# Performance work log

Measured on AMD Instinct MI355X. Metric: run time of the kernel, lower is better.

The kernel has to match this reference:

```python
import jax, jax.numpy as jnp
import numpy as np

S, N, LAT, HID, NH, NLAYERS = 8, 128, 128, 384, 8, 6
HT, WT, DT = 128, 128, 128
DIN, DOUT, RAD, LEVELS, FED = 1169, 3 + 3 * 128, 3, 4, 64


def sincos1d(d, pos):
    # MAE-style 1d sincos embedding, d even -> [..., d]
    omega = 1.0 / (10000.0 ** (jnp.arange(d // 2, dtype=jnp.float32) / (d / 2.0)))
    ang = pos[..., None] * omega
    return jnp.concatenate([jnp.sin(ang), jnp.cos(ang)], axis=-1)


def flow_embed(f, Cd=FED):
    # get_3d_embedding(flows, 64, cat_coords=True) -> [..., 3*Cd+3] = 195
    div = jnp.arange(0, Cd, 2, dtype=jnp.float32) * (1000.0 / Cd)
    outs = []
    for a in range(3):
        ang = f[..., a, None] * div
        pe = jnp.stack([jnp.sin(ang), jnp.cos(ang)], axis=-1).reshape(f.shape[:-1] + (Cd,))
        outs.append(pe)
    return jnp.concatenate(outs + [f], axis=-1)


def avg_pool2(x):
    B, Sv, Cc, H, W = x.shape
    return x.reshape(B, Sv, Cc, H // 2, 2, W // 2, 2).mean(axis=(4, 6))


def pyramid(fm):
    pyr = [fm]
    for _ in range(LEVELS - 1):
        fm = avg_pool2(fm)
        pyr.append(fm)
    return pyr


def bilinear_sample(corr, xy):
    # corr: [B,S,N,H,W]; xy: [B,S,N,P,2] pixel coords (x indexes W, y indexes H); zero padding
    B, Sv, Nn, H, W = corr.shape
    cf = corr.reshape(B, Sv, Nn, H * W)
    x, y = xy[..., 0], xy[..., 1]
    x0f = jnp.floor(x); y0f = jnp.floor(y)
    wx, wy = x - x0f, y - y0f
    x0 = x0f.astype(jnp.int32); y0 = y0f.astype(jnp.int32)

    def gather(xi, yi):
        ok = ((xi >= 0) & (xi < W) & (yi >= 0) & (yi < H)).astype(cf.dtype)
        idx = jnp.clip(yi, 0, H - 1) * W + jnp.clip(xi, 0, W - 1)
        v = jnp.take_along_axis(cf, idx.reshape(B, Sv, Nn, -1), axis=-1).reshape(idx.shape)
        return v * ok

    v00 = gather(x0, y0); v01 = gather(x0 + 1, y0)
    v10 = gather(x0, y0 + 1); v11 = gather(x0 + 1, y0 + 1)
    return v00 * (1 - wx) * (1 - wy) + v01 * wx * (1 - wy) + v10 * (1 - wx) * wy + v11 * wx * wy


def corr_sample(pyr, targets, coords):
    # RAFT/CoTracker CorrBlock: per-level dense correlation then (2r+1)^2 window bilinear lookup
    d = jnp.arange(-RAD, RAD + 1, dtype=jnp.float32)
    delta = jnp.stack(jnp.meshgrid(d, d, indexing="ij"), axis=-1).reshape(-1, 2)  # [49,2]
    scale = 1.0 / jnp.sqrt(jnp.float32(targets.shape[-1]))
    outs = []
    for l, fm in enumerate(pyr):
        corr = jnp.einsum("bsnc,bschw->bsnhw", targets, fm) * scale
        xy = coords[..., None, :] / (2.0 ** l) + delta
        outs.append(bilinear_sample(corr, xy))
    return jnp.concatenate(outs, axis=-1)  # [B,S,N,196]


def layernorm(x, g, b):
    m = x.mean(-1, keepdims=True)
    v = x.var(-1, keepdims=True)
    return (x - m) / jnp.sqrt(v + 1e-5) * g + b


def attention(x, Wqkv, bq, Wo, bo):
    M, T, H = x.shape
    dh = H // NH
    qkv = (x @ Wqkv + bq).reshape(M, T, 3, NH, dh)
    q, k, v = qkv[:, :, 0], qkv[:, :, 1], qkv[:, :, 2]
    att = jax.nn.softmax(jnp.einsum("mthd,mshd->mhts", q, k) / jnp.sqrt(jnp.float32(dh)), axis=-1)
    o = jnp.einsum("mhts,mshd->mthd", att, v).reshape(M, T, H)
    return o @ Wo + bo


def updateformer(x, support, W_in, b_in, lnp, Wqkv, bqkv, Wo, bo, W1, b1, W2, b2, W_out, b_out, Ws, bs):
    # x: [B,N,T,DIN]; alternating time (over T) and space (over N) pre-LN transformer blocks
    B, Np, T, _ = x.shape
    sproj = support @ Ws + bs  # [100,HID]
    h = x @ W_in + b_in + sproj.mean(axis=0)
    for i in range(NLAYERS):
        g1, bb1, g2, bb2 = lnp[i, 0], lnp[i, 1], lnp[i, 2], lnp[i, 3]
        if i % 2 == 0:
            y = h.reshape(B * Np, T, HID)
        else:
            y = h.transpose(0, 2, 1, 3).reshape(B * T, Np, HID)
        y = y + attention(layernorm(y, g1, bb1), Wqkv[i], bqkv[i], Wo[i], bo[i])
        z = layernorm(y, g2, bb2)
        y = y + jax.nn.gelu(z @ W1[i] + b1[i], approximate=False) @ W2[i] + b2[i]
        if i % 2 == 0:
            h = y.reshape(B, Np, T, HID)
        else:
            h = y.reshape(B, T, Np, HID).transpose(0, 2, 1, 3)
    return h @ W_out + b_out, sproj[None]


def groupnorm1(x, g, b):
    m = x.mean(-1, keepdims=True)
    v = x.var(-1, keepdims=True)
    return (x - m) / jnp.sqrt(v + 1e-5) * g + b


def _forward(fmapXY, fmapYZ, fmapXZ, coords_init, vis_init, track_mask, feat_init, support_features,
             W_in, b_in, lnp, Wqkv, bqkv, Wo, bo, W1, b1, W2, b2, W_out, b_out, Ws, bs,
             gn_g, gn_b, Wu, bu, Wvis, bvis, iters):
    B, Sv, Cc, H, W = fmapXY.shape
    D = fmapXZ.shape[-2]
    Nn = coords_init.shape[2]
    coords = coords_init
    ffeats = [feat_init[..., k] for k in range(3)]
    pyrXY, pyrYZ, pyrXZ = pyramid(fmapXY), pyramid(fmapYZ), pyramid(fmapXZ)
    grid_size = jnp.array([H, W, D], dtype=jnp.float32)
    # 3d sincos pos embed from query coords; 1169 padded to 1170 -> 390/axis, truncated back
    g = (coords[:, 0] / grid_size * 2.0 - 1.0) * 128.0  # [B,N,3]
    pe = jnp.concatenate([sincos1d(390, g[..., i]) for i in range(3)], axis=-1)[..., :DIN]
    pos_embed = pe.reshape(B * Nn, 1, DIN)
    times_embed = sincos1d(1170, jnp.arange(Sv, dtype=jnp.float32))[None, :, :DIN]
    support = support_features
    for _ in range(iters):
        coords = jax.lax.stop_gradient(coords)  # matches coords.detach()
        fxy = corr_sample(pyrXY, ffeats[0], coords[..., :2])
        fyz = corr_sample(pyrYZ, ffeats[1], coords[..., 1:3])
        fxz = corr_sample(pyrXZ, ffeats[2], coords[..., 0::2])
        fcorrs = jnp.concatenate([fxy, fyz, fxz], axis=-1)  # [B,S,N,588]
        fcorrs_ = fcorrs.transpose(0, 2, 1, 3).reshape(B * Nn, Sv, -1)
        flows_ = (coords - coords[:, :1]).transpose(0, 2, 1, 3).reshape(B * Nn, Sv, 3)
        flows_cat = flow_embed(flows_)  # [BN,S,195]
        ff = [f.transpose(0, 2, 1, 3).reshape(B * Nn, Sv, LAT) for f in ffeats]
        ffeats_ = jnp.concatenate(ff, axis=-1)  # [BN,S,384]
        # replicate torch's cat(dim=2)+permute+reshape layout exactly
        tmv = jnp.concatenate([track_mask, vis_init], axis=2).transpose(0, 2, 1, 3).reshape(B * Nn, Sv, 2)
        tin = jnp.concatenate([flows_cat, fcorrs_, ffeats_, tmv], axis=-1)  # [BN,S,1169]
        x = (tin + pos_embed + times_embed).reshape(B, Nn, Sv, DIN)
        delta, dse3 = updateformer(x, support, W_in, b_in, lnp, Wqkv, bqkv, Wo, bo, W1, b1, W2, b2, W_out, b_out, Ws, bs)
        support = support + dse3[0] / 100.0
        delta = delta.reshape(B * Nn, Sv, DOUT)
        d_coord = delta[..., :3].reshape(B, Nn, Sv, 3).transpose(0, 2, 1, 3)
        coords = coords + d_coord
        new_ffeats = []
        for k in range(3):
            dfk = delta[..., 3 + k * LAT:3 + (k + 1) * LAT]
            upd = jax.nn.gelu(groupnorm1(dfk, gn_g[k], gn_b[k]) @ Wu[k] + bu[k], approximate=False)
            new_ffeats.append(ffeats[k] + upd.reshape(B, Nn, Sv, LAT).transpose(0, 2, 1, 3))
        ffeats = new_ffeats
    vis = (jnp.concatenate(ffeats, axis=-1) @ Wvis + bvis)[..., 0]  # [B,S,N]
    return jnp.concatenate([coords, vis[..., None]], axis=-1)  # [B,S,N,4]


def setup_inputs() -> dict:
    key = jax.random.key(0)
    ks = jax.random.split(key, 16)
    f32 = jnp.float32
    B = 1
    fmapXY = jax.random.normal(ks[0], (B, S, LAT, HT, WT), f32)
    fmapYZ = jax.random.normal(ks[1], (B, S, LAT, DT, HT), f32)
    fmapXZ = jax.random.normal(ks[2], (B, S, LAT, DT, WT), f32)
    coords_init = jax.random.uniform(ks[3], (B, S, N, 3), f32) * 112.0 + 8.0
    vis_init = jnp.ones((B, S, N, 1), f32)
    track_mask = jnp.ones((B, S, N, 1), f32)
    feat_init = jax.random.normal(ks[4], (B, S, N, LAT, 3), f32)
    support_features = jnp.zeros((100, HID), f32) + 0.1
    w = lambda k, sh: jax.random.normal(k, sh, f32) * 0.02
    ln1 = jnp.stack([jnp.ones(HID, f32), jnp.zeros(HID, f32), jnp.ones(HID, f32), jnp.zeros(HID, f32)])
    params = dict(
        W_in=w(ks[5], (DIN, HID)), b_in=jnp.zeros((HID,), f32),
        lnp=jnp.tile(ln1[None], (NLAYERS, 1, 1)),
        Wqkv=w(ks[6], (NLAYERS, HID, 3 * HID)), bqkv=jnp.zeros((NLAYERS, 3 * HID), f32),
        Wo=w(ks[7], (NLAYERS, HID, HID)), bo=jnp.zeros((NLAYERS, HID), f32),
        W1=w(ks[8], (NLAYERS, HID, 4 * HID)), b1=jnp.zeros((NLAYERS, 4 * HID), f32),
        W2=w(ks[9], (NLAYERS, 4 * HID, HID)), b2=jnp.zeros((NLAYERS, HID), f32),
        W_out=w(ks[10], (HID, DOUT)), b_out=jnp.zeros((DOUT,), f32),
        Ws=w(ks[11], (HID, HID)), bs=jnp.zeros((HID,), f32),
        gn_g=jnp.ones((3, LAT), f32), gn_b=jnp.zeros((3, LAT), f32),
        Wu=w(ks[12], (3, LAT, LAT)), bu=jnp.zeros((3, LAT), f32),
        Wvis=w(ks[13], (3 * LAT, 1)), bvis=jnp.zeros((1,), f32),
    )
    return dict(fmapXY=fmapXY, fmapYZ=fmapYZ, fmapXZ=fmapXZ, coords_init=coords_init,
                vis_init=vis_init, track_mask=track_mask, feat_init=feat_init,
                support_features=support_features, iters=2, **params)


def reference(fmapXY, fmapYZ, fmapXZ, coords_init, vis_init, track_mask, feat_init, support_features,
              W_in, b_in, lnp, Wqkv, bqkv, Wo, bo, W1, b1, W2, b2, W_out, b_out, Ws, bs,
              gn_g, gn_b, Wu, bu, Wvis, bvis, iters):
    return _forward(fmapXY, fmapYZ, fmapXZ, coords_init, vis_init, track_mask, feat_init, support_features,
                    W_in, b_in, lnp, Wqkv, bqkv, Wo, bo, W1, b1, W2, b2, W_out, b_out, Ws, bs,
                    gn_g, gn_b, Wu, bu, Wvis, bvis, iters)
```

## Files before the change

kernel.cpp:

```cpp
#include <hip/hip_runtime.h>
#include <hip/hip_bf16.h>


#define DEVFN __device__ __forceinline__

typedef __attribute__((ext_vector_type(8))) short short8;
typedef __attribute__((ext_vector_type(4))) float f32x4;

static constexpr float INV_SQRT_DH = 0.14433756729740643f;
static constexpr float CORR_SCALE  = 0.08838834764831845f;
static constexpr size_t VSTRIDE = 22282240;

DEVFN float gelu_exact(float x){
  return 0.5f * x * (1.0f + erff(x * 0.7071067811865476f));
}
DEVFN short bf16_of(float f){
  __hip_bfloat16 b = __float2bfloat16(f);
  return *reinterpret_cast<short*>(&b);
}
DEVFN float bfu(uint32_t u16){ return __uint_as_float(u16 << 16); }
DEVFN float bf2f(__hip_bfloat16 b){ return __bfloat162float(b); }

DEVFN f32x4 MFMA(short8 a, short8 b, f32x4 c){
  return __builtin_amdgcn_mfma_f32_16x16x32_bf16(a,b,c,0,0,0);
}

template<int K, int MODE, bool AF32, int DEPTH>
static __device__ void mgemm_body(int bx, int by, const void* __restrict__ A, int lda,
                                  const __hip_bfloat16* __restrict__ Bt,
                                  float* __restrict__ C, int ldc,
                                  int M, int N, const float* __restrict__ bias, int tid){
  constexpr int NSTEP = K/32;
  int lane = tid & 63, wid = tid >> 6;
  int wr = wid >> 1, wc = wid & 1;
  int lr = lane & 15, lk = lane >> 4;
  int m0 = by*64 + wr*32;
  int n0 = bx*64 + wc*32;

  const __hip_bfloat16* Ab = (const __hip_bfloat16*)A;
  const float* Af = (const float*)A;
  size_t arow0 = (size_t)(m0 + lr)      * lda;
  size_t arow1 = (size_t)(m0 + 16 + lr) * lda;
  size_t brow0 = (size_t)(n0 + lr)      * K;
  size_t brow1 = (size_t)(n0 + 16 + lr) * K;

  auto loadA = [&](size_t ro, int k0)->short8{
    if constexpr (AF32){
      const float* p = Af + ro + k0 + lk*8;
      short8 r;
      #pragma unroll
      for (int j=0;j<8;j++) r[j] = bf16_of(p[j]);
      return r;
    } else {
      return *reinterpret_cast<const short8*>(Ab + ro + k0 + lk*8);
    }
  };
  auto loadB = [&](size_t ro, int k0)->short8{
    return *reinterpret_cast<const short8*>(Bt + ro + k0 + lk*8);
  };

  short8 a0[DEPTH], a1[DEPTH], b0[DEPTH], b1[DEPTH];
  #pragma unroll
  for (int p=0;p<DEPTH;p++){
    if (p < NSTEP){
      a0[p]=loadA(arow0,p*32); a1[p]=loadA(arow1,p*32);
      b0[p]=loadB(brow0,p*32); b1[p]=loadB(brow1,p*32);
    }
  }
  f32x4 acc00 = {}, acc01 = {}, acc10 = {}, acc11 = {};
  #pragma unroll
  for (int t=0;t<NSTEP;t++){
    const int cur = t % DEPTH;
    acc00 = MFMA(a0[cur],b0[cur],acc00);
    acc01 = MFMA(a0[cur],b1[cur],acc01);
    acc10 = MFMA(a1[cur],b0[cur],acc10);
    acc11 = MFMA(a1[cur],b1[cur],acc11);
    if (t+DEPTH < NSTEP){
      int k0 = (t+DEPTH)*32;
      a0[cur]=loadA(arow0,k0); a1[cur]=loadA(arow1,k0);
      b0[cur]=loadB(brow0,k0); b1[cur]=loadB(brow1,k0);
    }
  }

  f32x4 accs[2][2] = {{acc00, acc01},{acc10, acc11}};
  #pragma unroll
  for (int mi=0;mi<2;mi++){
    #pragma unroll
    for (int ni=0;ni<2;ni++){
      int c = n0 + ni*16 + lr;
      if (c >= N) continue;
      float bv = bias ? bias[c] : 0.0f;
      #pragma unroll
      for (int reg=0;reg<4;reg++){
        int r = m0 + mi*16 + lk*4 + reg;
        if (r >= M) continue;
        float v = accs[mi][ni][reg] + bv;
        if (MODE==0) C[(size_t)r*ldc + c] = v;
        else C[(size_t)r*ldc + c] += v;
      }
    }
  }
}

__global__ void init_all_k(float* coords, const float* cinit,
                           float* ff, const float* feat_init,
                           float* support, const float* sfeat,
                           float* posE, float* timE){
  int idx = blockIdx.x*256 + threadIdx.x;
  if (idx < 3072)  coords[idx]  = cinit[idx];
  if (idx < 49152){
    int row = idx / 384;
    support[idx] = (row < 100) ? sfeat[idx] : 0.0f;
  }
  if (idx < 393216){
    int k = idx / 131072, rest = idx % 131072;
    ff[idx] = feat_init[(size_t)rest*3 + k];
  }
  if (idx < 149632){
    int n = idx / 1169, d = idx % 1169;
    int i = d / 390, dd = d % 390;
    float c = cinit[n*3 + i];
    float g = (c / 128.0f * 2.0f - 1.0f) * 128.0f;
    int m = (dd < 195) ? dd : dd - 195;
    float om = powf(10000.0f, -(float)m / 195.0f);
    float ang = g * om;
    posE[idx] = (dd < 195) ? sinf(ang) : cosf(ang);
  }
  if (idx < 9352){
    int s = idx / 1169, d = idx % 1169;
    int m = (d < 585) ? d : d - 585;
    float om = powf(10000.0f, -(float)m / 585.0f);
    float ang = (float)s * om;
    timE[idx] = (d < 585) ? sinf(ang) : cosf(ang);
  }
}

__global__ void transpose_cl_k(const float* __restrict__ inXY, const float* __restrict__ inYZ,
                               const float* __restrict__ inXZ, __hip_bfloat16* __restrict__ pyr){
  __shared__ float tile[32][129];
  int v = blockIdx.z >> 3, s = blockIdx.z & 7;
  const float* in = (v==0) ? inXY : ((v==1) ? inYZ : inXZ);
  int c0 = blockIdx.y*32, h0 = blockIdx.x*128;
  int tx = threadIdx.x & 31, ty = threadIdx.x >> 5;
  const float* ib = in + (size_t)s*128*16384;
  #pragma unroll
  for (int r=0;r<4;r++){
    int c = c0 + ty + r*8;
    float4 f = *reinterpret_cast<const float4*>(ib + (size_t)c*16384 + h0 + tx*4);
    tile[ty+r*8][tx*4+0]=f.x; tile[ty+r*8][tx*4+1]=f.y;
    tile[ty+r*8][tx*4+2]=f.z; tile[ty+r*8][tx*4+3]=f.w;
  }
  __syncthreads();
  __hip_bfloat16* ob = pyr + (size_t)v*VSTRIDE + (size_t)s*16384*128;
  #pragma unroll
  for (int rr=0;rr<16;rr++){
    int hw = ty + rr*8;
    ob[(size_t)(h0+hw)*128 + c0 + tx] = __float2bfloat16(tile[tx][hw]);
  }
}

__global__ void pool2_k(__hip_bfloat16* __restrict__ pyr, size_t in_off, size_t out_off, int So){
  int idx = blockIdx.x*256 + threadIdx.x;
  int total = 8*So*So*128;
  if (idx >= total) return;
  const __hip_bfloat16* in = pyr + (size_t)blockIdx.z*VSTRIDE + in_off;
  __hip_bfloat16* out      = pyr + (size_t)blockIdx.z*VSTRIDE + out_off;
  int c = idx & 127;
  int x = (idx >> 7) % So;
  int y = ((idx >> 7) / So) % So;
  int s = idx / (So*So*128);
  int Si = So*2;
  const __hip_bfloat16* b0 = in + (((size_t)s*Si + 2*y)*Si + 2*x)*128 + c;
  float v = bf2f(b0[0]) + bf2f(b0[128])
          + bf2f(b0[(size_t)Si*128]) + bf2f(b0[(size_t)Si*128 + 128]);
  out[idx] = __float2bfloat16(v*0.25f);
}

__global__ void wtrans_all_k(const float* Ws, const float* W_in, const float* Wqkv,
                             const float* Wo, const float* W1, const float* W2,
                             const float* W_out, const float* Wu,
                             __hip_bfloat16* WsT, __hip_bfloat16* WinT, __hip_bfloat16* WqkvT,
                             __hip_bfloat16* WoT, __hip_bfloat16* W1T, __hip_bfloat16* W2T,
                             __hip_bfloat16* WoutT, __hip_bfloat16* WuT){
  __shared__ float tile[32][33];
  int z = blockIdx.z;
  const float* in; __hip_bfloat16* out; int K,N,Kp,Np;
  if (z==0){ in=Ws; out=WsT; K=384;N=384;Kp=384;Np=384; }
  else if (z==1){ in=W_in; out=WinT; K=1169;N=384;Kp=1184;Np=384; }
  else if (z<8){ int l=z-2; in=Wqkv+(size_t)l*442368; out=WqkvT+(size_t)l*442368; K=384;N=1152;Kp=384;Np=1152; }
  else if (z<14){ int l=z-8; in=Wo+(size_t)l*147456; out=WoT+(size_t)l*147456; K=384;N=384;Kp=384;Np=384; }
  else if (z<20){ int l=z-14; in=W1+(size_t)l*589824; out=W1T+(size_t)l*589824; K=384;N=1536;Kp=384;Np=1536; }
  else if (z<26){ int l=z-20; in=W2+(size_t)l*589824; out=W2T+(size_t)l*589824; K=1536;N=384;Kp=1536;Np=384; }
  else if (z==26){ in=W_out; out=WoutT; K=384;N=387;Kp=384;Np=448; }
  else { int l=z-27; in=Wu+(size_t)l*16384; out=WuT+(size_t)l*16384; K=128;N=128;Kp=128;Np=128; }
  int MK = (K>Kp)?K:Kp, MN = (N>Np)?N:Np;
  int kb = blockIdx.y*32, nb = blockIdx.x*32;
  if (kb >= MK || nb >= MN) return;
  int tx = threadIdx.x & 31, ty = threadIdx.x >> 5;
  #pragma unroll
  for (int r=0;r<4;r++){
    int k = kb + ty + r*8, n = nb + tx;
    tile[ty+r*8][tx] = (k < K && n < N) ? in[(size_t)k*N + n] : 0.0f;
  }
  __syncthreads();
  #pragma unroll
  for (int r=0;r<4;r++){
    int n = nb + ty + r*8, k = kb + tx;
    if (n < Np && k < Kp) out[(size_t)n*Kp + k] = __float2bfloat16(tile[tx][ty+r*8]);
  }
}

__global__ void assemble_x_k(__hip_bfloat16* __restrict__ xbuf, const float* __restrict__ posE,
                             const float* __restrict__ timE, const float* __restrict__ coords,
                             const float* __restrict__ ff, const float* __restrict__ tmask,
                             const float* __restrict__ vinit,
                             const float* __restrict__ support,
                             const __hip_bfloat16* __restrict__ WsT,
                             float* __restrict__ sproj, const float* __restrict__ bs){
  if (blockIdx.x >= 1024){
    int b = blockIdx.x - 1024;
    mgemm_body<384,0,true,3>(b%6, b/6, support,384, WsT, sproj,384, 100,384, bs, threadIdx.x);
    return;
  }
  int r = blockIdx.x;
  int n = r >> 3, s = r & 7;
  for (int d = threadIdx.x; d < 1184; d += blockDim.x){
    __hip_bfloat16* dst = xbuf + (size_t)r*1184 + d;
    if (d >= 1169){ *dst = __float2bfloat16(0.0f); continue; }
    float base = posE[(size_t)n*1169 + d] + timE[(size_t)s*1169 + d];
    if (d >= 195 && d < 783){ *dst = __float2bfloat16(base); continue; }
    float val;
    if (d < 195){
      if (d >= 192){
        int a = d - 192;
        val = coords[(s*128+n)*3 + a] - coords[n*3 + a];
      } else {
        int a = d >> 6, dd = d & 63;
        float f = coords[(s*128+n)*3 + a] - coords[n*3 + a];
        float ang = f * (31.25f * (float)(dd >> 1));
        val = (dd & 1) ? cosf(ang) : sinf(ang);
      }
    } else if (d < 1167){
      int cidx = d - 783, k = cidx >> 7, cc = cidx & 127;
      val = ff[(size_t)k*131072 + (size_t)(s*128+n)*128 + cc];
    } else {
      int c = d - 1167;
      int flat = n*16 + s*2 + c;
      int n2 = flat >> 3, s2 = flat & 7;
      val = (n2 < 128) ? tmask[s2*128 + n2] : vinit[s2*128 + (n2-128)];
    }
    *dst = __float2bfloat16(val + base);
  }
}

__global__ void corr_k(const __hip_bfloat16* __restrict__ pyr, const float* __restrict__ coords,
                       const float* __restrict__ ff, __hip_bfloat16* __restrict__ xbuf,
                       const float* __restrict__ sproj, const float* __restrict__ b_in,
                       float* __restrict__ bias2, float* __restrict__ support){
  if (blockIdx.x >= 3072){
    int idx = (blockIdx.x - 3072)*256 + threadIdx.x;
    if (idx < 38400) support[idx] += sproj[idx]*0.01f;
    else if (idx < 38784){
      int c = idx - 38400;
      float s = 0.0f;
      for (int r=0;r<100;r++) s += sproj[r*384 + c];
      bias2[c] = b_in[c] + s*0.01f;
    }
    return;
  }
  __shared__ float t[128];
  __shared__ float p[4][64];
  int bid = blockIdx.x;
  int view = bid >> 10, s = (bid >> 7) & 7, n = bid & 127;
  int tid = threadIdx.x;
  int l = tid >> 6, t64 = tid & 63;
  if (tid < 128) t[tid] = ff[(size_t)view*131072 + (size_t)(s*128+n)*128 + tid];
  int ax = (view==1) ? 1 : 0;
  int ay = (view==0) ? 1 : 2;
  float X = coords[(s*128+n)*3 + ax];
  float Y = coords[(s*128+n)*3 + ay];
  const __hip_bfloat16* vb = pyr + (size_t)view*VSTRIDE;
  __syncthreads();

  int sz = 128 >> l;
  size_t loff = (l==0) ? 0ull : (l==1 ? 16777216ull : (l==2 ? 20971520ull : 22020096ull));
  float inv = 1.0f / (float)(1 << l);
  float cx = X * inv, cy = Y * inv;
  float x0f = floorf(cx), y0f = floorf(cy);
  float wx = cx - x0f, wy = cy - y0f;
  int ix0 = (int)x0f, iy0 = (int)y0f;
  int px = ix0 - 3 + (t64 & 7);
  int py = iy0 - 3 + (t64 >> 3);
  float acc = 0.0f;
  if (px >= 0 && px < sz && py >= 0 && py < sz){
    const uint2* row = reinterpret_cast<const uint2*>(vb + loff + (((size_t)s*sz + py)*sz + px)*128);
    #pragma unroll
    for (int c4=0;c4<32;c4++){
      uint2 u = row[c4];
      float f0 = __uint_as_float(u.x << 16);
      float f1 = __uint_as_float(u.x & 0xffff0000u);
      float f2 = __uint_as_float(u.y << 16);
      float f3 = __uint_as_float(u.y & 0xffff0000u);
      acc += t[c4*4+0]*f0 + t[c4*4+1]*f1 + t[c4*4+2]*f2 + t[c4*4+3]*f3;
    }
  }
  p[l][t64] = acc;
  __syncthreads();
  if (t64 < 49){
    int i = t64 / 7, jj = t64 % 7;
    float v = p[l][jj*8+i]       * (1.0f-wx)*(1.0f-wy)
            + p[l][jj*8+i+1]     * wx*(1.0f-wy)
            + p[l][(jj+1)*8+i]   * (1.0f-wx)*wy
            + p[l][(jj+1)*8+i+1] * wx*wy;
    __hip_bfloat16* dst = xbuf + (size_t)(n*8+s)*1184 + 195 + view*196 + l*49 + t64;
    *dst = __float2bfloat16(__bfloat162float(*dst) + v * CORR_SCALE);
  }
}

__global__ void gn_rows_k(const float* __restrict__ dbuf,
                          const float* __restrict__ gn_g, const float* __restrict__ gn_b,
                          __hip_bfloat16* __restrict__ gtmp, float* __restrict__ coords){
  int k = blockIdx.y;
  const float* in = dbuf + 3 + k*128;
  const float* g = gn_g + k*128;
  const float* b = gn_b + k*128;
  __hip_bfloat16* out = gtmp + (size_t)k*131072;
  int wave = threadIdx.x >> 6, lane = threadIdx.x & 63;
  int r = blockIdx.x*4 + wave;
  const float* row = in + (size_t)r*387;
  float x0 = row[lane], x1 = row[lane+64];
  float sum = x0 + x1;
  #pragma unroll
  for (int o=32;o>0;o>>=1) sum += __shfl_xor(sum, o);
  float mean = sum / 128.0f;
  float d0 = x0-mean, d1 = x1-mean;
  float vs = d0*d0 + d1*d1;
  #pragma unroll
  for (int o=32;o>0;o>>=1) vs += __shfl_xor(vs, o);
  float invstd = 1.0f / sqrtf(vs/128.0f + 1e-5f);
  out[(size_t)r*128 + lane]      = __float2bfloat16(d0*invstd*g[lane] + b[lane]);
  out[(size_t)r*128 + lane + 64] = __float2bfloat16(d1*invstd*g[lane+64] + b[lane+64]);
  if (k == 0 && blockIdx.x < 12){
    int idx = blockIdx.x*256 + threadIdx.x;
    if (idx < 3072){
      int a = idx % 3, sn = idx / 3;
      int ss = sn >> 7, nn = sn & 127;
      coords[idx] += dbuf[(size_t)(nn*8+ss)*387 + a];
    }
  }
}

template<int K, int MODE, bool AF32, int DEPTH>
__global__ __launch_bounds__(256) void mgemm_k(const void* __restrict__ A, int lda,
                                               const __hip_bfloat16* __restrict__ Bt,
                                               float* __restrict__ C, int ldc,
                                               int M, int N,
                                               const float* __restrict__ bias){
  mgemm_body<K,MODE,AF32,DEPTH>(blockIdx.x, blockIdx.y, A, lda, Bt, C, ldc, M, N, bias, threadIdx.x);
}

__global__ __launch_bounds__(256) void ln_qkv_k(const float* __restrict__ A,
                                                const float* __restrict__ gamma,
                                                const float* __restrict__ beta,
                                                const __hip_bfloat16* __restrict__ Bt,
                                                __hip_bfloat16* __restrict__ Cbf,
                                                const float* __restrict__ bias){
  constexpr int LDSS = 392;
  __shared__ short Asm[64*LDSS];
  int tid = threadIdx.x, lane = tid & 63, w = tid >> 6;
  int m0 = blockIdx.y*64, n0b = blockIdx.x*128;

  float gg[6], bb[6];
  #pragma unroll
  for (int e=0;e<6;e++){ gg[e] = gamma[lane+e*64]; bb[e] = beta[lane+e*64]; }
  for (int rr=0; rr<16; rr++){
    int r = w*16 + rr;
    const float* row = A + (size_t)(m0+r)*384;
    float x[6]; float sum = 0.0f;
    #pragma unroll
    for (int e=0;e<6;e++){ x[e] = row[lane+e*64]; sum += x[e]; }
    #pragma unroll
    for (int o=32;o>0;o>>=1) sum += __shfl_xor(sum, o);
    float mean = sum * (1.0f/384.0f);
    float vs = 0.0f;
    #pragma unroll
    for (int e=0;e<6;e++){ float d = x[e]-mean; vs += d*d; }
    #pragma unroll
    for (int o=32;o>0;o>>=1) vs += __shfl_xor(vs, o);
    float invstd = 1.0f / sqrtf(vs*(1.0f/384.0f) + 1e-5f);
    #pragma unroll
    for (int e=0;e<6;e++)
      Asm[r*LDSS + lane + e*64] = bf16_of((x[e]-mean)*invstd*gg[e] + bb[e]);
  }
  __syncthreads();

  int wr = w >> 1, wc = w & 1;
  int lr = lane & 15, lk = lane >> 4;
  const __hip_bfloat16* Brow[4];
  #pragma unroll
  for (int ni=0;ni<4;ni++) Brow[ni] = Bt + (size_t)(n0b + wc*64 + ni*16 + lr)*384;

  short8 bfrag[4][4];
  #pragma unroll
  for (int p=0;p<4;p++)
    #pragma unroll
    for (int ni=0;ni<4;ni++)
      bfrag[p][ni] = *(const short8*)(Brow[ni] + p*32 + lk*8);

  f32x4 acc[2][4] = {};
  #pragma unroll
  for (int t=0;t<12;t++){
    const int cur = t & 3;
    short8 a0 = *(const short8*)(&Asm[(wr*32+lr)*LDSS    + t*32 + lk*8]);
    short8 a1 = *(const short8*)(&Asm[(wr*32+16+lr)*LDSS + t*32 + lk*8]);
    #pragma unroll
    for (int ni=0;ni<4;ni++){
      acc[0][ni] = MFMA(a0,bfrag[cur][ni],acc[0][ni]);
      acc[1][ni] = MFMA(a1,bfrag[cur][ni],acc[1][ni]);
    }
    if (t+4 < 12){
      #pragma unroll
      for (int ni=0;ni<4;ni++)
        bfrag[cur][ni] = *(const short8*)(Brow[ni] + (t+4)*32 + lk*8);
    }
  }
  #pragma unroll
  for (int mi=0;mi<2;mi++){
    #pragma unroll
    for (int ni=0;ni<4;ni++){
      int c = n0b + wc*64 + ni*16 + lr;
      float bv = bias[c];
      #pragma unroll
      for (int reg=0;reg<4;reg++){
        int r = m0 + wr*32 + mi*16 + lk*4 + reg;
        Cbf[(size_t)r*1152 + c] = __float2bfloat16(acc[mi][ni][reg] + bv);
      }
    }
  }
}

template<bool GELU>
__global__ __launch_bounds__(256) void lngemm_k(const float* __restrict__ A,
                                                const float* __restrict__ gamma,
                                                const float* __restrict__ beta,
                                                const __hip_bfloat16* __restrict__ Bt,
                                                __hip_bfloat16* __restrict__ Cbf, int ldc,
                                                const float* __restrict__ bias){
  constexpr int LDSS = 392;
  __shared__ short Asm[64*LDSS];
  int tid = threadIdx.x, lane = tid & 63, w = tid >> 6;
  int m0 = blockIdx.y*64, n0b = blockIdx.x*128;

  float gg[6], bb[6];
  #pragma unroll
  for (int e=0;e<6;e++){ gg[e] = gamma[lane+e*64]; bb[e] = beta[lane+e*64]; }
  for (int rr=0; rr<16; rr++){
    int r = w*16 + rr;
    const float* row = A + (size_t)(m0+r)*384;
    float x[6]; float sum = 0.0f;
    #pragma unroll
    for (int e=0;e<6;e++){ x[e] = row[lane+e*64]; sum += x[e]; }
    #pragma unroll
    for (int o=32;o>0;o>>=1) sum += __shfl_xor(sum, o);
    float mean = sum * (1.0f/384.0f);
    float vs = 0.0f;
    #pragma unroll
    for (int e=0;e<6;e++){ float d = x[e]-mean; vs += d*d; }
    #pragma unroll
    for (int o=32;o>0;o>>=1) vs += __shfl_xor(vs, o);
    float invstd = 1.0f / sqrtf(vs*(1.0f/384.0f) + 1e-5f);
    #pragma unroll
    for (int e=0;e<6;e++)
      Asm[r*LDSS + lane + e*64] = bf16_of((x[e]-mean)*invstd*gg[e] + bb[e]);
  }
  __syncthreads();

  int wr = w >> 1, wc = w & 1;
  int lr = lane & 15, lk = lane >> 4;
  const __hip_bfloat16* Brow[4];
  #pragma unroll
  for (int ni=0;ni<4;ni++) Brow[ni] = Bt + (size_t)(n0b + wc*64 + ni*16 + lr)*384;

  short8 bfrag[2][4];
  #pragma unroll
  for (int p=0;p<2;p++)
    #pragma unroll
    for (int ni=0;ni<4;ni++)
      bfrag[p][ni] = *(const short8*)(Brow[ni] + p*32 + lk*8);

  f32x4 acc[2][4] = {};
  #pragma unroll
  for (int t=0;t<12;t++){
    const int cur = t & 1;
    short8 a0 = *(const short8*)(&Asm[(wr*32+lr)*LDSS    + t*32 + lk*8]);
    short8 a1 = *(const short8*)(&Asm[(wr*32+16+lr)*LDSS + t*32 + lk*8]);
    #pragma unroll
    for (int ni=0;ni<4;ni++){
      acc[0][ni] = MFMA(a0,bfrag[cur][ni],acc[0][ni]);
      acc[1][ni] = MFMA(a1,bfrag[cur][ni],acc[1][ni]);
    }
    if (t+2 < 12){
      #pragma unroll
      for (int ni=0;ni<4;ni++)
        bfrag[cur][ni] = *(const short8*)(Brow[ni] + (t+2)*32 + lk*8);
    }
  }
  #pragma unroll
  for (int mi=0;mi<2;mi++){
    #pragma unroll
    for (int ni=0;ni<4;ni++){
      int c = n0b + wc*64 + ni*16 + lr;
      float bv = bias[c];
      #pragma unroll
      for (int reg=0;reg<4;reg++){
        int r = m0 + wr*32 + mi*16 + lk*4 + reg;
        float v = acc[mi][ni][reg] + bv;
        Cbf[(size_t)r*ldc + c] = __float2bfloat16(GELU ? gelu_exact(v) : v);
      }
    }
  }
}

__global__ __launch_bounds__(256) void wu_gemm_k(const __hip_bfloat16* __restrict__ gtmp,
                                                 const __hip_bfloat16* __restrict__ WuT,
                                                 const float* __restrict__ bu,
                                                 float* __restrict__ ff){
  int z = blockIdx.z;
  const __hip_bfloat16* A  = gtmp + (size_t)z*131072;
  const __hip_bfloat16* Bt = WuT  + (size_t)z*16384;
  const float* bias = bu + (size_t)z*128;
  float* aux = ff + (size_t)z*131072;
  int tid = threadIdx.x, lane = tid & 63, wid = tid >> 6;
  int wr = wid >> 1, wc = wid & 1;
  int lr = lane & 15, lk = lane >> 4;
  int m0 = blockIdx.y*64 + wr*32;
  int n0 = blockIdx.x*64 + wc*32;
  const short8* A0 = (const short8*)(A + (size_t)(m0+lr)*128);
  const short8* A1 = (const short8*)(A + (size_t)(m0+16+lr)*128);
  const short8* B0 = (const short8*)(Bt + (size_t)(n0+lr)*128);
  const short8* B1 = (const short8*)(Bt + (size_t)(n0+16+lr)*128);
  f32x4 acc00={}, acc01={}, acc10={}, acc11={};
  #pragma unroll
  for (int t=0;t<4;t++){
    short8 a0 = A0[t*4 + lk], a1 = A1[t*4 + lk];
    short8 b0 = B0[t*4 + lk], b1 = B1[t*4 + lk];
    acc00 = MFMA(a0,b0,acc00);
    acc01 = MFMA(a0,b1,acc01);
    acc10 = MFMA(a1,b0,acc10);
    acc11 = MFMA(a1,b1,acc11);
  }
  f32x4 accs[2][2] = {{acc00, acc01},{acc10, acc11}};
  #pragma unroll
  for (int mi=0;mi<2;mi++){
    #pragma unroll
    for (int ni=0;ni<2;ni++){
      int c = n0 + ni*16 + lr;
      float bv = bias[c];
      #pragma unroll
      for (int reg=0;reg<4;reg++){
        int r = m0 + mi*16 + lk*4 + reg;
        float v = accs[mi][ni][reg] + bv;
        int ss = r & 7, nn2 = r >> 3;
        aux[((size_t)(ss*128+nn2))*128 + c] += gelu_exact(v);
      }
    }
  }
}

__global__ __launch_bounds__(512) void attn_even_k(const __hip_bfloat16* __restrict__ qkv,
                                                   __hip_bfloat16* __restrict__ attout){
  int g = blockIdx.x;
  int h = threadIdx.x >> 6;
  int lane = threadIdx.x & 63;
  int t = lane >> 3, j = lane & 7;
  const short* qs = (const short*)qkv;

  float q[48], kk[48];
  {
    const short8* qp = (const short8*)(qs + (size_t)(g*8+t)*1152 + h*48);
    const short8* kp = (const short8*)(qs + (size_t)(g*8+j)*1152 + 384 + h*48);
    #pragma unroll
    for (int c=0;c<6;c++){
      short8 qv = qp[c], kv = kp[c];
      #pragma unroll
      for (int e=0;e<8;e++){
        q[c*8+e]  = bfu((uint16_t)qv[e]);
        kk[c*8+e] = bfu((uint16_t)kv[e]);
      }
    }
  }
  float s = 0.0f;
  #pragma unroll
  for (int d=0;d<48;d++) s += q[d]*kk[d];
  s *= INV_SQRT_DH;
  float mx = s;
  #pragma unroll
  for (int o=1;o<8;o<<=1) mx = fmaxf(mx, __shfl_xor(mx, o));
  float e = expf(s - mx);
  float l = e;
  #pragma unroll
  for (int o=1;o<8;o<<=1) l += __shfl_xor(l, o);
  float p = e / l;

  float o6[6] = {0,0,0,0,0,0};
  #pragma unroll
  for (int jp=0;jp<8;jp++){
    float pj = __shfl(p, (lane & 56) | jp);
    const uint32_t* vp = (const uint32_t*)(qs + (size_t)(g*8+jp)*1152 + 768 + h*48 + j*6);
    uint32_t w0 = vp[0], w1 = vp[1], w2 = vp[2];
    o6[0] += pj * bfu(w0 & 0xffffu); o6[1] += pj * bfu(w0 >> 16);
    o6[2] += pj * bfu(w1 & 0xffffu); o6[3] += pj * bfu(w1 >> 16);
    o6[4] += pj * bfu(w2 & 0xffffu); o6[5] += pj * bfu(w2 >> 16);
  }
  uint32_t r0 = ((uint32_t)(uint16_t)bf16_of(o6[1]) << 16) | (uint16_t)bf16_of(o6[0]);
  uint32_t r1 = ((uint32_t)(uint16_t)bf16_of(o6[3]) << 16) | (uint16_t)bf16_of(o6[2]);
  uint32_t r2 = ((uint32_t)(uint16_t)bf16_of(o6[5]) << 16) | (uint16_t)bf16_of(o6[4]);
  uint32_t* op = (uint32_t*)((short*)attout + (size_t)(g*8+t)*384 + h*48 + j*6);
  op[0] = r0; op[1] = r1; op[2] = r2;
}

__global__ __launch_bounds__(256) void attn_odd_mfma_k(const __hip_bfloat16* __restrict__ qkv,
                                                       __hip_bfloat16* __restrict__ attout){
  __shared__ char smem[47872];
  short* Qb = (short*)smem;
  short* Kb = (short*)(smem + 18432);
  short* Pb = (short*)smem;
  short* Vt = (short*)(smem + 34816);
  int g = blockIdx.x & 7, h = blockIdx.x >> 3;
  int tid = threadIdx.x;

  const short* qs = (const short*)qkv;
  for (int idx = tid; idx < 768; idx += 256){
    int t = idx / 6, dblk = idx % 6;
    size_t base = (size_t)(t*8+g)*1152 + h*48 + dblk*8;
    *(short8*)(Qb + t*72 + dblk*8) = *(const short8*)(qs + base);
    *(short8*)(Kb + t*72 + dblk*8) = *(const short8*)(qs + base + 384);
  }
  short8 zz = {};
  for (int idx = tid; idx < 384; idx += 256){
    int t = idx / 3, dblk = idx % 3;
    *(short8*)(Qb + t*72 + 48 + dblk*8) = zz;
    *(short8*)(Kb + t*72 + 48 + dblk*8) = zz;
  }
  __syncthreads();

  int lane = tid & 63, w = tid >> 6;
  int lr = lane & 15, lk = lane >> 4;
  int m0 = w*32;

  f32x4 S[2][8] = {};
  #pragma unroll
  for (int ks=0; ks<2; ks++){
    short8 a0 = *(const short8*)(Qb + (m0+lr)*72    + ks*32 + lk*8);
    short8 a1 = *(const short8*)(Qb + (m0+16+lr)*72 + ks*32 + lk*8);
    #pragma unroll
    for (int ni=0; ni<8; ni++){
      short8 b = *(const short8*)(Kb + (ni*16+lr)*72 + ks*32 + lk*8);
      S[0][ni] = MFMA(a0,b,S[0][ni]);
      S[1][ni] = MFMA(a1,b,S[1][ni]);
    }
  }

  #pragma unroll
  for (int mi=0;mi<2;mi++){
    #pragma unroll
    for (int reg=0;reg<4;reg++){
      float m = -1e30f;
      #pragma unroll
      for (int ni=0;ni<8;ni++) m = fmaxf(m, S[mi][ni][reg]);
      #pragma unroll
      for (int o=1;o<16;o<<=1) m = fmaxf(m, __shfl_xor(m, o));
      m *= INV_SQRT_DH;
      float l = 0.0f;
      #pragma unroll
      for (int ni=0;ni<8;ni++){
        float p = expf(S[mi][ni][reg]*INV_SQRT_DH - m);
        S[mi][ni][reg] = p;
        l += p;
      }
      #pragma unroll
      for (int o=1;o<16;o<<=1) l += __shfl_xor(l, o);
      float inv = 1.0f/l;
      #pragma unroll
      for (int ni=0;ni<8;ni++) S[mi][ni][reg] *= inv;
    }
  }
  __syncthreads();

  for (int idx = tid; idx < 768; idx += 256){
    int j = idx / 6, dblk = idx % 6;
    short8 v = *(const short8*)(qs + (size_t)(j*8+g)*1152 + 768 + h*48 + dblk*8);
    #pragma unroll
    for (int e=0;e<8;e++) Vt[(dblk*8+e)*136 + j] = v[e];
  }
  #pragma unroll
  for (int mi=0;mi<2;mi++)
    #pragma unroll
    for (int ni=0;ni<8;ni++)
      #pragma unroll
      for (int reg=0;reg<4;reg++)
        Pb[(m0+mi*16+lk*4+reg)*136 + ni*16+lr] = bf16_of(S[mi][ni][reg]);
  __syncthreads();

  f32x4 O[2][3] = {};
  #pragma unroll
  for (int ks=0; ks<4; ks++){
    short8 a0 = *(const short8*)(Pb + (m0+lr)*136    + ks*32 + lk*8);
    short8 a1 = *(const short8*)(Pb + (m0+16+lr)*136 + ks*32 + lk*8);
    #pragma unroll
    for (int ni=0; ni<3; ni++){
      short8 b = *(const short8*)(Vt + (ni*16+lr)*136 + ks*32 + lk*8);
      O[0][ni] = MFMA(a0,b,O[0][ni]);
      O[1][ni] = MFMA(a1,b,O[1][ni]);
    }
  }
  #pragma unroll
  for (int mi=0;mi<2;mi++){
    #pragma unroll
    for (int ni=0;ni<3;ni++){
      #pragma unroll
      for (int reg=0;reg<4;reg++){
        int q = m0 + mi*16 + lk*4 + reg;
        int d = ni*16 + lr;
        attout[(size_t)(q*8+g)*384 + h*48 + d] = __float2bfloat16(O[mi][ni][reg]);
      }
    }
  }
}

__global__ void final_out_k(const float* __restrict__ coords, const float* __restrict__ ff,
                            const float* __restrict__ Wvis, const float* __restrict__ bvis,
                            float* __restrict__ out){
  int sn = blockIdx.x*64 + threadIdx.x;
  if (sn >= 1024) return;
  float acc = bvis[0];
  for (int k=0;k<3;k++)
    for (int c=0;c<128;c++)
      acc += ff[(size_t)k*131072 + (size_t)sn*128 + c] * Wvis[k*128 + c];
  out[sn*4+0] = coords[sn*3+0];
  out[sn*4+1] = coords[sn*3+1];
  out[sn*4+2] = coords[sn*3+2];
  out[sn*4+3] = acc;
}


extern "C" void kernel_launch(void* const* d_in, const int* in_sizes, int n_in,
                              void* d_out, int out_size, void* d_ws, size_t ws_size,
                              hipStream_t stream) {
  const float* fmapXY   = (const float*)d_in[0];
  const float* fmapYZ   = (const float*)d_in[1];
  const float* fmapXZ   = (const float*)d_in[2];
  const float* cinit    = (const float*)d_in[3];
  const float* vinit    = (const float*)d_in[4];
  const float* tmask    = (const float*)d_in[5];
  const float* feat_init= (const float*)d_in[6];
  const float* sfeat    = (const float*)d_in[7];
  const float* W_in     = (const float*)d_in[9];
  const float* b_in     = (const float*)d_in[10];
  const float* lnp      = (const float*)d_in[11];
  const float* Wqkv     = (const float*)d_in[12];
  const float* bqkv     = (const float*)d_in[13];
  const float* Wo       = (const float*)d_in[14];
  const float* bo       = (const float*)d_in[15];
  const float* W1       = (const float*)d_in[16];
  const float* b1       = (const float*)d_in[17];
  const float* W2       = (const float*)d_in[18];
  const float* b2       = (const float*)d_in[19];
  const float* W_out    = (const float*)d_in[20];
  const float* b_out    = (const float*)d_in[21];
  const float* Ws       = (const float*)d_in[22];
  const float* bs       = (const float*)d_in[23];
  const float* gn_g     = (const float*)d_in[24];
  const float* gn_b     = (const float*)d_in[25];
  const float* Wu       = (const float*)d_in[26];
  const float* bu       = (const float*)d_in[27];
  const float* Wvis     = (const float*)d_in[28];
  const float* bvis     = (const float*)d_in[29];
  const int ITERS = 2;

  char* wp = (char*)d_ws;
  auto alloc = [&](size_t bytes)->char* {
    char* p = wp; wp += (bytes + 255) & ~(size_t)255; return p;
  };
  __hip_bfloat16* pyr = (__hip_bfloat16*)alloc(3ull*VSTRIDE*2);
  float* coords = (float*)alloc(3072ull*4);
  float* ff     = (float*)alloc(393216ull*4);
  float* support= (float*)alloc(49152ull*4);
  float* sproj  = (float*)alloc(38400ull*4);
  float* bias2  = (float*)alloc(384ull*4);
  float* posE   = (float*)alloc(149632ull*4);
  float* timE   = (float*)alloc(9352ull*4);
  float* hbuf   = (float*)alloc(393216ull*4);
  float* dbuf   = (float*)alloc(396288ull*4);
  __hip_bfloat16* xbuf_bf = (__hip_bfloat16*)alloc(1212416ull*2);
  __hip_bfloat16* qkv_bf  = (__hip_bfloat16*)alloc(1179648ull*2);
  __hip_bfloat16* atto_bf = (__hip_bfloat16*)alloc(393216ull*2);
  __hip_bfloat16* ffb_bf  = (__hip_bfloat16*)alloc(1572864ull*2);
  __hip_bfloat16* gtmp_bf = (__hip_bfloat16*)alloc(393216ull*2);
  __hip_bfloat16* WsT   = (__hip_bfloat16*)alloc(147456ull*2);
  __hip_bfloat16* WinT  = (__hip_bfloat16*)alloc(454656ull*2);
  __hip_bfloat16* WqkvT = (__hip_bfloat16*)alloc(2654208ull*2);
  __hip_bfloat16* WoT   = (__hip_bfloat16*)alloc(884736ull*2);
  __hip_bfloat16* W1T   = (__hip_bfloat16*)alloc(3538944ull*2);
  __hip_bfloat16* W2T   = (__hip_bfloat16*)alloc(3538944ull*2);
  __hip_bfloat16* WoutT = (__hip_bfloat16*)alloc(172032ull*2);
  __hip_bfloat16* WuT   = (__hip_bfloat16*)alloc(49152ull*2);
  if ((size_t)(wp - (char*)d_ws) > ws_size) return;

  init_all_k<<<1536, 256, 0, stream>>>(coords, cinit, ff, feat_init, support, sfeat, posE, timE);
  transpose_cl_k<<<dim3(128,4,24), 256, 0, stream>>>(fmapXY, fmapYZ, fmapXZ, pyr);
  pool2_k<<<dim3((8*64*64*128 + 255)/256,1,3), 256, 0, stream>>>(pyr, 0,        16777216, 64);
  pool2_k<<<dim3((8*32*32*128 + 255)/256,1,3), 256, 0, stream>>>(pyr, 16777216, 20971520, 32);
  pool2_k<<<dim3((8*16*16*128 + 255)/256,1,3), 256, 0, stream>>>(pyr, 20971520, 22020096, 16);
  wtrans_all_k<<<dim3(48,48,30), 256, 0, stream>>>(Ws, W_in, Wqkv, Wo, W1, W2, W_out, Wu,
                                                   WsT, WinT, WqkvT, WoT, W1T, W2T, WoutT, WuT);

  for (int it=0; it<ITERS; ++it){
    assemble_x_k<<<1036, 256, 0, stream>>>(xbuf_bf, posE, timE, coords, ff, tmask, vinit,
                                           support, WsT, sproj, bs);
    corr_k<<<3224, 256, 0, stream>>>(pyr, coords, ff, xbuf_bf, sproj, b_in, bias2, support);

    mgemm_k<1184,0,false,6><<<dim3(6,16), 256, 0, stream>>>(xbuf_bf,1184, WinT, hbuf,384, 1024,384, bias2);

    for (int i=0;i<6;i++){
      const float* g1  = lnp + (size_t)(i*4+0)*384;
      const float* bb1 = lnp + (size_t)(i*4+1)*384;
      const float* g2  = lnp + (size_t)(i*4+2)*384;
      const float* bb2 = lnp + (size_t)(i*4+3)*384;

      ln_qkv_k<<<dim3(9,16), 256, 0, stream>>>(hbuf, g1, bb1, WqkvT + (size_t)i*442368,
                                               qkv_bf, bqkv + i*1152);
      if ((i & 1) == 0) attn_even_k<<<128, 512, 0, stream>>>(qkv_bf, atto_bf);
      else              attn_odd_mfma_k<<<64, 256, 0, stream>>>(qkv_bf, atto_bf);
      mgemm_k<384,1,false,3><<<dim3(6,16), 256, 0, stream>>>(atto_bf,384, WoT + (size_t)i*147456,
                                                             hbuf,384, 1024,384, bo + i*384);
      lngemm_k<true><<<dim3(12,16), 256, 0, stream>>>(hbuf, g2, bb2, W1T + (size_t)i*589824,
                                                      ffb_bf, 1536, b1 + i*1536);
      mgemm_k<1536,1,false,6><<<dim3(6,16), 256, 0, stream>>>(ffb_bf,1536, W2T + (size_t)i*589824,
                                                              hbuf,384, 1024,384, b2 + i*384);
    }

    mgemm_k<384,0,true,3><<<dim3(7,16), 256, 0, stream>>>(hbuf,384, WoutT, dbuf,387, 1024,387, b_out);
    gn_rows_k<<<dim3(256,3), 256, 0, stream>>>(dbuf, gn_g, gn_b, gtmp_bf, coords);
    wu_gemm_k<<<dim3(2,16,3), 256, 0, stream>>>(gtmp_bf, WuT, bu, ff);
  }

  final_out_k<<<16, 64, 0, stream>>>(coords, ff, Wvis, bvis, (float*)d_out);
}
```

Measured before the change: 1.440 ms.

## Fuse init into transpose kernel and groupnorm into Wu GEMM

```diff
diff --git a/kernel.cpp b/kernel.cpp
--- a/kernel.cpp
+++ b/kernel.cpp
@@ -102,60 +102,68 @@
   }
 }
 
-__global__ void init_all_k(float* coords, const float* cinit,
-                           float* ff, const float* feat_init,
-                           float* support, const float* sfeat,
-                           float* posE, float* timE){
-  int idx = blockIdx.x*256 + threadIdx.x;
-  if (idx < 3072)  coords[idx]  = cinit[idx];
-  if (idx < 49152){
-    int row = idx / 384;
-    support[idx] = (row < 100) ? sfeat[idx] : 0.0f;
-  }
-  if (idx < 393216){
-    int k = idx / 131072, rest = idx % 131072;
-    ff[idx] = feat_init[(size_t)rest*3 + k];
-  }
-  if (idx < 149632){
-    int n = idx / 1169, d = idx % 1169;
-    int i = d / 390, dd = d % 390;
-    float c = cinit[n*3 + i];
-    float g = (c / 128.0f * 2.0f - 1.0f) * 128.0f;
-    int m = (dd < 195) ? dd : dd - 195;
-    float om = powf(10000.0f, -(float)m / 195.0f);
-    float ang = g * om;
-    posE[idx] = (dd < 195) ? sinf(ang) : cosf(ang);
-  }
-  if (idx < 9352){
-    int s = idx / 1169, d = idx % 1169;
-    int m = (d < 585) ? d : d - 585;
-    float om = powf(10000.0f, -(float)m / 585.0f);
-    float ang = (float)s * om;
-    timE[idx] = (d < 585) ? sinf(ang) : cosf(ang);
-  }
-}
-
-__global__ void transpose_cl_k(const float* __restrict__ inXY, const float* __restrict__ inYZ,
-                               const float* __restrict__ inXZ, __hip_bfloat16* __restrict__ pyr){
-  __shared__ float tile[32][129];
-  int v = blockIdx.z >> 3, s = blockIdx.z & 7;
+__global__ void transpose_init_k(const float* __restrict__ inXY, const float* __restrict__ inYZ,
+                                 const float* __restrict__ inXZ, __hip_bfloat16* __restrict__ pyr,
+                                 float* coords, const float* cinit,
+                                 float* ff, const float* feat_init,
+                                 float* support, const float* sfeat,
+                                 float* posE, float* timE){
+  int bid = blockIdx.x;
+  int tid = threadIdx.x;
+  if (bid >= 12288){
+    int idx = (bid - 12288)*256 + tid;
+    if (idx < 3072)  coords[idx]  = cinit[idx];
+    if (idx < 49152){
+      int row = idx / 384;
+      support[idx] = (row < 100) ? sfeat[idx] : 0.0f;
+    }
+    if (idx < 393216){
+      int k = idx / 131072, rest = idx % 131072;
+      ff[idx] = feat_init[(size_t)rest*3 + k];
+    }
+    if (idx < 149632){
+      int n = idx / 1169, d = idx % 1169;
+      int i = d / 390, dd = d % 390;
+      float c = cinit[n*3 + i];
+      float g = (c / 128.0f * 2.0f - 1.0f) * 128.0f;
+      int m = (dd < 195) ? dd : dd - 195;
+      float om = powf(10000.0f, -(float)m / 195.0f);
+      float ang = g * om;
+      posE[idx] = (dd < 195) ? sinf(ang) : cosf(ang);
+    }
+    if (idx < 9352){
+      int s = idx / 1169, d = idx % 1169;
+      int m = (d < 585) ? d : d - 585;
+      float om = powf(10000.0f, -(float)m / 585.0f);
+      float ang = (float)s * om;
+      timE[idx] = (d < 585) ? sinf(ang) : cosf(ang);
+    }
+    return;
+  }
+  __shared__ float tile[128][33];
+  int vz = bid >> 9;
+  int v = vz >> 3, s = vz & 7;
   const float* in = (v==0) ? inXY : ((v==1) ? inYZ : inXZ);
-  int c0 = blockIdx.y*32, h0 = blockIdx.x*128;
-  int tx = threadIdx.x & 31, ty = threadIdx.x >> 5;
+  int h0 = (bid & 511) * 32;
   const float* ib = in + (size_t)s*128*16384;
+  int chunk = tid & 7;
+  int cbase = tid >> 3;
   #pragma unroll
   for (int r=0;r<4;r++){
-    int c = c0 + ty + r*8;
-    float4 f = *reinterpret_cast<const float4*>(ib + (size_t)c*16384 + h0 + tx*4);
-    tile[ty+r*8][tx*4+0]=f.x; tile[ty+r*8][tx*4+1]=f.y;
-    tile[ty+r*8][tx*4+2]=f.z; tile[ty+r*8][tx*4+3]=f.w;
+    int c = cbase + r*32;
+    float4 f = *reinterpret_cast<const float4*>(ib + (size_t)c*16384 + h0 + chunk*4);
+    tile[c][chunk*4+0]=f.x; tile[c][chunk*4+1]=f.y;
+    tile[c][chunk*4+2]=f.z; tile[c][chunk*4+3]=f.w;
   }
   __syncthreads();
   __hip_bfloat16* ob = pyr + (size_t)v*VSTRIDE + (size_t)s*16384*128;
-  #pragma unroll
-  for (int rr=0;rr<16;rr++){
-    int hw = ty + rr*8;
-    ob[(size_t)(h0+hw)*128 + c0 + tx] = __float2bfloat16(tile[tx][hw]);
+  int w = tid >> 6, lane = tid & 63;
+  #pragma unroll
+  for (int rr=0;rr<8;rr++){
+    int hw = w*8 + rr;
+    uint32_t lo = (uint32_t)(uint16_t)bf16_of(tile[2*lane][hw]);
+    uint32_t hi = (uint32_t)(uint16_t)bf16_of(tile[2*lane+1][hw]);
+    reinterpret_cast<uint32_t*>(ob + (size_t)(h0+hw)*128)[lane] = lo | (hi<<16);
   }
 }
 
@@ -317,39 +325,6 @@
   }
 }
 
-__global__ void gn_rows_k(const float* __restrict__ dbuf,
-                          const float* __restrict__ gn_g, const float* __restrict__ gn_b,
-                          __hip_bfloat16* __restrict__ gtmp, float* __restrict__ coords){
-  int k = blockIdx.y;
-  const float* in = dbuf + 3 + k*128;
-  const float* g = gn_g + k*128;
-  const float* b = gn_b + k*128;
-  __hip_bfloat16* out = gtmp + (size_t)k*131072;
-  int wave = threadIdx.x >> 6, lane = threadIdx.x & 63;
-  int r = blockIdx.x*4 + wave;
-  const float* row = in + (size_t)r*387;
-  float x0 = row[lane], x1 = row[lane+64];
-  float sum = x0 + x1;
-  #pragma unroll
-  for (int o=32;o>0;o>>=1) sum += __shfl_xor(sum, o);
-  float mean = sum / 128.0f;
-  float d0 = x0-mean, d1 = x1-mean;
-  float vs = d0*d0 + d1*d1;
-  #pragma unroll
-  for (int o=32;o>0;o>>=1) vs += __shfl_xor(vs, o);
-  float invstd = 1.0f / sqrtf(vs/128.0f + 1e-5f);
-  out[(size_t)r*128 + lane]      = __float2bfloat16(d0*invstd*g[lane] + b[lane]);
-  out[(size_t)r*128 + lane + 64] = __float2bfloat16(d1*invstd*g[lane+64] + b[lane+64]);
-  if (k == 0 && blockIdx.x < 12){
-    int idx = blockIdx.x*256 + threadIdx.x;
-    if (idx < 3072){
-      int a = idx % 3, sn = idx / 3;
-      int ss = sn >> 7, nn = sn & 127;
-      coords[idx] += dbuf[(size_t)(nn*8+ss)*387 + a];
-    }
-  }
-}
-
 template<int K, int MODE, bool AF32, int DEPTH>
 __global__ __launch_bounds__(256) void mgemm_k(const void* __restrict__ A, int lda,
                                                const __hip_bfloat16* __restrict__ Bt,
@@ -521,29 +496,59 @@
   }
 }
 
-__global__ __launch_bounds__(256) void wu_gemm_k(const __hip_bfloat16* __restrict__ gtmp,
-                                                 const __hip_bfloat16* __restrict__ WuT,
-                                                 const float* __restrict__ bu,
-                                                 float* __restrict__ ff){
-  int z = blockIdx.z;
-  const __hip_bfloat16* A  = gtmp + (size_t)z*131072;
-  const __hip_bfloat16* Bt = WuT  + (size_t)z*16384;
+__global__ __launch_bounds__(256) void gn_wu_k(const float* __restrict__ dbuf,
+                                               const float* __restrict__ gn_g,
+                                               const float* __restrict__ gn_b,
+                                               const __hip_bfloat16* __restrict__ WuT,
+                                               const float* __restrict__ bu,
+                                               float* __restrict__ ff,
+                                               float* __restrict__ coords){
+  __shared__ short Asm[64*136];
+  int z = blockIdx.z, by = blockIdx.y, bx = blockIdx.x;
+  int tid = threadIdx.x, lane = tid & 63, w = tid >> 6;
+  const float* g = gn_g + z*128;
+  const float* b = gn_b + z*128;
+
+  for (int rr=0; rr<16; ++rr){
+    int r = w*16 + rr;
+    const float* row = dbuf + (size_t)(by*64 + r)*387 + 3 + z*128;
+    float x0 = row[lane], x1 = row[lane+64];
+    float sum = x0 + x1;
+    #pragma unroll
+    for (int o=32;o>0;o>>=1) sum += __shfl_xor(sum, o);
+    float mean = sum * (1.0f/128.0f);
+    float d0 = x0-mean, d1 = x1-mean;
+    float vs = d0*d0 + d1*d1;
+    #pragma unroll
+    for (int o=32;o>0;o>>=1) vs += __shfl_xor(vs, o);
+    float invstd = 1.0f / sqrtf(vs*(1.0f/128.0f) + 1e-5f);
+    Asm[r*136 + lane]      = bf16_of(d0*invstd*g[lane] + b[lane]);
+    Asm[r*136 + lane + 64] = bf16_of(d1*invstd*g[lane+64] + b[lane+64]);
+  }
+  if (z == 0 && bx == 0 && by < 12){
+    int idx = by*256 + tid;
+    if (idx < 3072){
+      int a = idx % 3, sn = idx / 3;
+      int ss = sn >> 7, nn = sn & 127;
+      coords[idx] += dbuf[(size_t)(nn*8+ss)*387 + a];
+    }
+  }
+  __syncthreads();
+
+  int wr = w >> 1, wc = w & 1;
+  int lr = lane & 15, lk = lane >> 4;
+  int m0l = wr*32;
+  int n0 = bx*64 + wc*32;
+  const __hip_bfloat16* Bt = WuT + (size_t)z*16384;
   const float* bias = bu + (size_t)z*128;
   float* aux = ff + (size_t)z*131072;
-  int tid = threadIdx.x, lane = tid & 63, wid = tid >> 6;
-  int wr = wid >> 1, wc = wid & 1;
-  int lr = lane & 15, lk = lane >> 4;
-  int m0 = blockIdx.y*64 + wr*32;
-  int n0 = blockIdx.x*64 + wc*32;
-  const short8* A0 = (const short8*)(A + (size_t)(m0+lr)*128);
-  const short8* A1 = (const short8*)(A + (size_t)(m0+16+lr)*128);
-  const short8* B0 = (const short8*)(Bt + (size_t)(n0+lr)*128);
-  const short8* B1 = (const short8*)(Bt + (size_t)(n0+16+lr)*128);
   f32x4 acc00={}, acc01={}, acc10={}, acc11={};
   #pragma unroll
   for (int t=0;t<4;t++){
-    short8 a0 = A0[t*4 + lk], a1 = A1[t*4 + lk];
-    short8 b0 = B0[t*4 + lk], b1 = B1[t*4 + lk];
+    short8 a0 = *(const short8*)(&Asm[(m0l+lr)*136    + t*32 + lk*8]);
+    short8 a1 = *(const short8*)(&Asm[(m0l+16+lr)*136 + t*32 + lk*8]);
+    short8 b0 = *(const short8*)(Bt + (size_t)(n0+lr)*128    + t*32 + lk*8);
+    short8 b1 = *(const short8*)(Bt + (size_t)(n0+16+lr)*128 + t*32 + lk*8);
     acc00 = MFMA(a0,b0,acc00);
     acc01 = MFMA(a0,b1,acc01);
     acc10 = MFMA(a1,b0,acc10);
@@ -558,7 +563,7 @@
       float bv = bias[c];
       #pragma unroll
       for (int reg=0;reg<4;reg++){
-        int r = m0 + mi*16 + lk*4 + reg;
+        int r = by*64 + m0l + mi*16 + lk*4 + reg;
         float v = accs[mi][ni][reg] + bv;
         int ss = r & 7, nn2 = r >> 3;
         aux[((size_t)(ss*128+nn2))*128 + c] += gelu_exact(v);
@@ -796,7 +801,6 @@
   __hip_bfloat16* qkv_bf  = (__hip_bfloat16*)alloc(1179648ull*2);
   __hip_bfloat16* atto_bf = (__hip_bfloat16*)alloc(393216ull*2);
   __hip_bfloat16* ffb_bf  = (__hip_bfloat16*)alloc(1572864ull*2);
-  __hip_bfloat16* gtmp_bf = (__hip_bfloat16*)alloc(393216ull*2);
   __hip_bfloat16* WsT   = (__hip_bfloat16*)alloc(147456ull*2);
   __hip_bfloat16* WinT  = (__hip_bfloat16*)alloc(454656ull*2);
   __hip_bfloat16* WqkvT = (__hip_bfloat16*)alloc(2654208ull*2);
@@ -807,8 +811,9 @@
   __hip_bfloat16* WuT   = (__hip_bfloat16*)alloc(49152ull*2);
   if ((size_t)(wp - (char*)d_ws) > ws_size) return;
 
-  init_all_k<<<1536, 256, 0, stream>>>(coords, cinit, ff, feat_init, support, sfeat, posE, timE);
-  transpose_cl_k<<<dim3(128,4,24), 256, 0, stream>>>(fmapXY, fmapYZ, fmapXZ, pyr);
+  transpose_init_k<<<13824, 256, 0, stream>>>(fmapXY, fmapYZ, fmapXZ, pyr,
+                                              coords, cinit, ff, feat_init,
+                                              support, sfeat, posE, timE);
   pool2_k<<<dim3((8*64*64*128 + 255)/256,1,3), 256, 0, stream>>>(pyr, 0,        16777216, 64);
   pool2_k<<<dim3((8*32*32*128 + 255)/256,1,3), 256, 0, stream>>>(pyr, 16777216, 20971520, 32);
   pool2_k<<<dim3((8*16*16*128 + 255)/256,1,3), 256, 0, stream>>>(pyr, 20971520, 22020096, 16);
@@ -841,8 +846,7 @@
     }
 
     mgemm_k<384,0,true,3><<<dim3(7,16), 256, 0, stream>>>(hbuf,384, WoutT, dbuf,387, 1024,387, b_out);
-    gn_rows_k<<<dim3(256,3), 256, 0, stream>>>(dbuf, gn_g, gn_b, gtmp_bf, coords);
-    wu_gemm_k<<<dim3(2,16,3), 256, 0, stream>>>(gtmp_bf, WuT, bu, ff);
+    gn_wu_k<<<dim3(2,16,3), 256, 0, stream>>>(dbuf, gn_g, gn_b, WuT, bu, ff, coords);
   }
 
   final_out_k<<<16, 64, 0, stream>>>(coords, ff, Wvis, bvis, (float*)d_out);
```

Result: no change. 1.455 ms (+1.0%).
